# Kernel tuning notes

Measured on AMD Instinct MI355X. Metric: run time of the kernel, lower is better.

Reference implementation:

```python
import jax, jax.numpy as jnp
import numpy as np

KSIZE = 7
STRIDE = 4
SCALE = 10.0
C_IN = 64
C_INT = 16
TOP_M = 100


def _unfold(x, k, s):
    # x: [B,C,H,W] -> [B, C*k*k, L] with torch.nn.Unfold channel ordering (c, ki, kj)
    B, C, H, W = x.shape
    oh = (H - k) // s + 1
    ow = (W - k) // s + 1
    rows = jnp.arange(oh)[:, None] * s + jnp.arange(k)[None, :]  # [oh,k]
    cols = jnp.arange(ow)[:, None] * s + jnp.arange(k)[None, :]  # [ow,k]
    p = x[:, :, rows][:, :, :, :, cols]          # [B,C,oh,k,ow,k]
    p = p.transpose(0, 1, 3, 5, 2, 4)            # [B,C,k,k,oh,ow]
    return p.reshape(B, C * k * k, oh * ow)


def _fold(p, H, W, k, s):
    # inverse of _unfold with overlap-add (torch.nn.Fold semantics)
    B, D, L = p.shape
    C = D // (k * k)
    oh = (H - k) // s + 1
    ow = (W - k) // s + 1
    rows = jnp.arange(oh)[:, None] * s + jnp.arange(k)[None, :]
    cols = jnp.arange(ow)[:, None] * s + jnp.arange(k)[None, :]
    p = p.reshape(B, C, k, k, oh, ow).transpose(0, 1, 4, 2, 5, 3)  # [B,C,oh,k,ow,k]
    out = jnp.zeros((B, C, H, W), p.dtype)
    return out.at[:, :, rows[:, :, None, None], cols[None, None, :, :]].add(p)


def _conv1x1(x, w, b):
    return jnp.einsum('bchw,oc->bohw', x, w) + b[None, :, None, None]


def _conv3x3(x, w, b):
    y = jax.lax.conv_general_dilated(x, w, (1, 1), ((1, 1), (1, 1)),
                                     dimension_numbers=('NCHW', 'OIHW', 'NCHW'))
    return y + b[None, :, None, None]


def setup_inputs() -> dict:
    key = jax.random.key(0)
    ks = jax.random.split(key, 12)
    B, H, W = 4, 127, 127
    s = 0.05  # small init std keeps softmax logits in a sane range
    return {
        'x': jax.random.normal(ks[0], (B, C_IN, H, W), jnp.float32),
        'g_w': jax.random.normal(ks[1], (C_INT, C_IN, 3, 3), jnp.float32) * s,
        'g_b': jnp.zeros((C_INT,), jnp.float32),
        'theta_w': jax.random.normal(ks[2], (C_INT, C_IN), jnp.float32) * s,
        'theta_b': jnp.zeros((C_INT,), jnp.float32),
        'phi_w': jax.random.normal(ks[3], (C_INT, C_IN), jnp.float32) * s,
        'phi_b': jnp.zeros((C_INT,), jnp.float32),
        'match_w': jax.random.normal(ks[4], (C_INT, C_IN), jnp.float32) * s,
        'match_b': jnp.zeros((C_INT,), jnp.float32),
        'restore_w': jax.random.normal(ks[5], (C_IN, C_INT), jnp.float32) * s,
        'restore_b': jnp.zeros((C_IN,), jnp.float32),
    }


def reference(x, g_w, g_b, theta_w, theta_b, phi_w, phi_b,
              match_w, match_b, restore_w, restore_b):
    B, C, H, W = x.shape
    b1 = _conv3x3(x, g_w, g_b)           # [B,16,H,W]
    b2 = _conv1x1(x, theta_w, theta_b)
    b3 = _conv1x1(x, phi_w, phi_b)

    p1 = _unfold(b1, KSIZE, STRIDE).transpose(0, 2, 1)  # [B,L,D], D=16*49
    p2 = _unfold(b2, KSIZE, STRIDE).transpose(0, 2, 1)
    p3 = _unfold(b3, KSIZE, STRIDE).transpose(0, 2, 1)

    score = jnp.einsum('bld,bmd->blm', p1, p2)           # [B,L,L]
    L = score.shape[-1]
    k = min(TOP_M, L)
    vals, idx = jax.lax.top_k(score, k)                  # [B,L,k]
    bI = jnp.arange(B)[:, None, None]
    rI = jnp.arange(L)[None, :, None]
    sparse = jnp.zeros_like(score).at[bI, rI, idx].set(vals)
    attn = jax.nn.softmax(sparse * SCALE, axis=-1)

    agg = jnp.einsum('blm,bmd->bld', attn, p3).transpose(0, 2, 1)  # [B,D,L]
    out = _fold(agg, H, W, KSIZE, STRIDE)                # [B,16,H,W]

    mask = _fold(_unfold(jnp.ones_like(x), KSIZE, STRIDE), H, W, KSIZE, STRIDE)
    mask = _conv1x1(mask, match_w, match_b)              # [B,16,H,W]

    out = out / (mask + 1e-8)
    out = _conv1x1(out, restore_w, restore_b)            # [B,64,H,W]
    return out
```

## Files before the change

### kernel.cpp

```cpp
#include <hip/hip_runtime.h>
#include <hip/hip_bf16.h>

typedef __hip_bfloat16 bf16;
typedef unsigned short ushort_t;
typedef __attribute__((ext_vector_type(8))) __bf16 bfv8;
typedef __attribute__((ext_vector_type(16))) float f32x16;

#define B_   4
#define CIN  64
#define CI   16
#define H_   127
#define W_   127
#define HW   (H_*W_)
#define KS   7
#define ST   4
#define OH_  31
#define L_   961
#define D_   784
#define TOPM 100

#define N1   1032256
#define WG_O 4
#define WT_O (WG_O + 9216)
#define WP_O (WT_O + 1024)
#define BG_O (WP_O + 1024)
#define BT_O (BG_O + 16)
#define BP_O (BT_O + 16)
#define SM_O (BP_O + 16)
#define SB_O (SM_O + 16)
#define RW_O (SB_O + 16)
#define RB_O (RW_O + 1024)
#define B1_O 12448
#define S3_O (B1_O + 3*N1)
#define WB_O (S3_O + B_*D_)
#define REG_O (WB_O + 36864)
#define XHSZ 4129024
#define SROW 964
#define SCSLOT 926464
#define AGSZ 753424
#define TKROW 112
#define SLST 72
#define PKPLANE 753424
#define PKSTR   1506848

#define FULL_BYTES ((size_t)(REG_O + XHSZ + 4*AGSZ) * 4)
#define MID_BYTES  ((size_t)(REG_O + XHSZ) * 4)

__device__ __forceinline__ float bf2f(bf16 v) { return __bfloat162float(v); }
__device__ __forceinline__ float bflo(unsigned u) { return __uint_as_float(u << 16); }
__device__ __forceinline__ float bfhi(unsigned u) { return __uint_as_float(u & 0xFFFF0000u); }

template <typename T> struct Ld;
template <> struct Ld<float> {
  static __device__ __forceinline__ float f(const void* p, int i) { return ((const float*)p)[i]; }
};
template <> struct Ld<bf16> {
  static __device__ __forceinline__ float f(const void* p, int i) { return bf2f(((const bf16*)p)[i]); }
};

__device__ __forceinline__ unsigned fmap(float f) {
  unsigned u = __float_as_uint(f);
  return (u & 0x80000000u) ? ~u : (u | 0x80000000u);
}
__device__ __forceinline__ float unfmap(unsigned kk) {
  unsigned u = (kk & 0x80000000u) ? (kk & 0x7fffffffu) : ~kk;
  return __uint_as_float(u);
}

__device__ __forceinline__ ushort_t f2bf(float x) {
  unsigned u = __float_as_uint(x);
  return (ushort_t)((u + 0x7FFFu + ((u >> 16) & 1u)) >> 16);
}
__device__ __forceinline__ void splitbf(float x, ushort_t& h, ushort_t& l) {
  h = f2bf(x);
  float hf = __uint_as_float(((unsigned)h) << 16);
  l = f2bf(x - hf);
}

__global__ void k_detect(const unsigned short* __restrict__ xh, int* __restrict__ flag) {
  int tid = threadIdx.x;
  int c = 0;
#pragma unroll
  for (int j = 0; j < 2; ++j) {
    unsigned u = xh[tid * 2 + j];
    unsigned e = (u >> 7) & 0xFF;
    if (e >= 134) c++;
  }
#pragma unroll
  for (int o = 32; o; o >>= 1) c += __shfl_down(c, o);
  if (tid == 0) *flag = (c >= 8) ? 1 : 0;
}

#define LDW(ptr, i) (f ? ((const float*)(ptr))[i] : bf2f(((const bf16*)(ptr))[i]))
__global__ __launch_bounds__(256) void k_prep(
    const int* __restrict__ flag,
    const void* g_w, const void* t_w, const void* p_w,
    const void* g_b, const void* t_b, const void* p_b,
    const void* m_w, const void* m_b, const void* r_w, const void* r_b,
    float* __restrict__ ws)
{
  int f = *flag;
  int gid = blockIdx.x * 256 + threadIdx.x;
  int gs = gridDim.x * 256;
  for (int i = gid; i < 9216; i += gs) {
    int o = i & 15, t = i >> 4, c = t & 63, tap = t >> 6;
    ws[WG_O + i] = LDW(g_w, (o * 64 + c) * 9 + tap);
  }
  for (int i = gid; i < 1024; i += gs) {
    int o = i & 15, c = i >> 4;
    ws[WT_O + i] = LDW(t_w, o * 64 + c);
    ws[WP_O + i] = LDW(p_w, o * 64 + c);
  }
  if (gid < 16) {
    ws[BG_O + gid] = LDW(g_b, gid);
    ws[BT_O + gid] = LDW(t_b, gid);
    ws[BP_O + gid] = LDW(p_b, gid);
    float s = 0.f;
    for (int c = 0; c < 64; ++c) s += LDW(m_w, gid * 64 + c);
    ws[SM_O + gid] = s;
    ws[SB_O + gid] = LDW(m_b, gid);
  }
  for (int i = gid; i < 1024; i += gs) ws[RW_O + i] = LDW(r_w, i);
  if (gid >= 64 && gid < 128) ws[RB_O + gid - 64] = LDW(r_b, gid - 64);
  ushort_t* wBh = (ushort_t*)(ws + WB_O);
  ushort_t* wBl = wBh + 9 * 64 * 64;
  for (int i = gid; i < 9 * 64 * 64; i += gs) {
    int c = i & 63, t = i >> 6, col = t & 63, tap = t >> 6;
    float v = 0.f;
    if (col < 16) v = LDW(g_w, (col * 64 + c) * 9 + tap);
    else if (col < 32) { if (tap == 4) v = LDW(t_w, (col - 16) * 64 + c); }
    else if (col < 48) { if (tap == 4) v = LDW(p_w, (col - 32) * 64 + c); }
    ushort_t h, l; splitbf(v, h, l);
    wBh[i] = h; wBl[i] = l;
  }
}

__global__ __launch_bounds__(256) void k_hwc(
    const int* __restrict__ flag, const void* __restrict__ x,
    ushort_t* __restrict__ xhh, ushort_t* __restrict__ xhl)
{
  __shared__ float tile[64][65];
  int pix0 = blockIdx.x * 64;
  int tid = threadIdx.x;
  int g = tid >> 6, p = tid & 63;
  int pix = pix0 + p;
  bool ok = pix < B_ * HW;
  int bb = ok ? pix / HW : 0;
  int r  = ok ? pix - bb * HW : 0;
  if (*flag) {
    const float* xf = (const float*)x;
    for (int c = g * 16; c < g * 16 + 16; ++c)
      tile[p][c] = ok ? xf[((size_t)bb * CIN + c) * HW + r] : 0.f;
  } else {
    const bf16* xb = (const bf16*)x;
    for (int c = g * 16; c < g * 16 + 16; ++c)
      tile[p][c] = ok ? bf2f(xb[((size_t)bb * CIN + c) * HW + r]) : 0.f;
  }
  __syncthreads();
  int c2 = tid & 63, pg = tid >> 6;
  for (int k = 0; k < 16; ++k) {
    int p2 = pg * 16 + k;
    int pix2 = pix0 + p2;
    if (pix2 < B_ * HW) {
      ushort_t h, l; splitbf(tile[p2][c2], h, l);
      xhh[(size_t)pix2 * 64 + c2] = h;
      xhl[(size_t)pix2 * 64 + c2] = l;
    }
  }
}

__global__ __launch_bounds__(256) void k_conv3(
    const float* __restrict__ ws,
    const ushort_t* __restrict__ xhh, const ushort_t* __restrict__ xhl,
    ushort_t* __restrict__ b1h, ushort_t* __restrict__ b1l,
    ushort_t* __restrict__ b2h, ushort_t* __restrict__ b2l,
    ushort_t* __restrict__ b3)
{
  __shared__ ushort_t sAh[128 * SLST], sAl[128 * SLST];
  __shared__ ushort_t sBh[64 * SLST],  sBl[64 * SLST];
  int bz = blockIdx.z;
  int px0 = blockIdx.x * 128;
  int tid = threadIdx.x, lane = tid & 63, wv = tid >> 6;

  int pix0 = px0 + lane, pix1 = px0 + lane + 64;
  bool pok0 = pix0 < HW, pok1 = pix1 < HW;
  int ph0 = pok0 ? pix0 / W_ : 0, pw0 = pok0 ? pix0 - ph0 * W_ : 0;
  int ph1 = pok1 ? pix1 / W_ : 0, pw1 = pok1 ? pix1 - ph1 * W_ : 0;
  const ushort_t* xplane = ((wv == 0) ? xhh : xhl) + (size_t)bz * HW * 64;
  const ushort_t* wBh_ = (const ushort_t*)(ws + WB_O);
  const ushort_t* bsrc = (wv == 2) ? wBh_ : (wBh_ + 9 * 64 * 64);
  ushort_t* dplane = (wv == 0) ? sAh : (wv == 1) ? sAl : (wv == 2) ? sBh : sBl;
  ushort_t* drow0 = dplane + lane * SLST;
  ushort_t* drow1 = dplane + (lane + 64) * SLST;

  int fr = lane & 31, kh = (lane >> 5) << 3;
  int mt = (wv >> 1) << 1;
  int aoff0 = (mt * 32 + fr) * SLST + kh;
  int aoff1 = ((mt + 1) * 32 + fr) * SLST + kh;
  int boff  = (((wv & 1) << 5) + fr) * SLST + kh;

  f32x16 acc0 = {0.f,0.f,0.f,0.f,0.f,0.f,0.f,0.f,0.f,0.f,0.f,0.f,0.f,0.f,0.f,0.f};
  f32x16 acc1 = {0.f,0.f,0.f,0.f,0.f,0.f,0.f,0.f,0.f,0.f,0.f,0.f,0.f,0.f,0.f,0.f};
  const int4 z4 = make_int4(0, 0, 0, 0);
  int4 v0 = z4, v1 = z4, v2 = z4, v3 = z4, v4 = z4, v5 = z4, v6 = z4, v7 = z4;
  int4 u0 = z4, u1 = z4, u2 = z4, u3 = z4, u4 = z4, u5 = z4, u6 = z4, u7 = z4;

  if (wv < 2) {
    int hh = ph0 - 1, ww = pw0 - 1;
    if (pok0 && hh >= 0 && ww >= 0) {
      const int4* s = (const int4*)(xplane + (size_t)(hh * W_ + ww) * 64);
      v0 = s[0]; v1 = s[1]; v2 = s[2]; v3 = s[3]; v4 = s[4]; v5 = s[5]; v6 = s[6]; v7 = s[7];
    }
    int hh1 = ph1 - 1, ww1 = pw1 - 1;
    if (pok1 && hh1 >= 0 && ww1 >= 0) {
      const int4* s = (const int4*)(xplane + (size_t)(hh1 * W_ + ww1) * 64);
      u0 = s[0]; u1 = s[1]; u2 = s[2]; u3 = s[3]; u4 = s[4]; u5 = s[5]; u6 = s[6]; u7 = s[7];
    }
  } else {
    const int4* s = (const int4*)(bsrc + (size_t)lane * 64);
    v0 = s[0]; v1 = s[1]; v2 = s[2]; v3 = s[3]; v4 = s[4]; v5 = s[5]; v6 = s[6]; v7 = s[7];
  }

  for (int r = 0; r < 9; ++r) {
    __syncthreads();
    *(int4*)(drow0 + 0)  = v0;  *(int4*)(drow0 + 8)  = v1;
    *(int4*)(drow0 + 16) = v2;  *(int4*)(drow0 + 24) = v3;
    *(int4*)(drow0 + 32) = v4;  *(int4*)(drow0 + 40) = v5;
    *(int4*)(drow0 + 48) = v6;  *(int4*)(drow0 + 56) = v7;
    if (wv < 2) {
      *(int4*)(drow1 + 0)  = u0;  *(int4*)(drow1 + 8)  = u1;
      *(int4*)(drow1 + 16) = u2;  *(int4*)(drow1 + 24) = u3;
      *(int4*)(drow1 + 32) = u4;  *(int4*)(drow1 + 40) = u5;
      *(int4*)(drow1 + 48) = u6;  *(int4*)(drow1 + 56) = u7;
    }
    __syncthreads();
    if (r < 8) {
      int rn = r + 1;
      int dh = rn / 3 - 1, dw = rn % 3 - 1;
      if (wv < 2) {
        int hh = ph0 + dh, ww = pw0 + dw;
        if (pok0 && (unsigned)hh < (unsigned)H_ && (unsigned)ww < (unsigned)W_) {
          const int4* s = (const int4*)(xplane + (size_t)(hh * W_ + ww) * 64);
          v0 = s[0]; v1 = s[1]; v2 = s[2]; v3 = s[3]; v4 = s[4]; v5 = s[5]; v6 = s[6]; v7 = s[7];
        } else {
          v0 = z4; v1 = z4; v2 = z4; v3 = z4; v4 = z4; v5 = z4; v6 = z4; v7 = z4;
        }
        int hh1 = ph1 + dh, ww1 = pw1 + dw;
        if (pok1 && (unsigned)hh1 < (unsigned)H_ && (unsigned)ww1 < (unsigned)W_) {
          const int4* s = (const int4*)(xplane + (size_t)(hh1 * W_ + ww1) * 64);
          u0 = s[0]; u1 = s[1]; u2 = s[2]; u3 = s[3]; u4 = s[4]; u5 = s[5]; u6 = s[6]; u7 = s[7];
        } else {
          u0 = z4; u1 = z4; u2 = z4; u3 = z4; u4 = z4; u5 = z4; u6 = z4; u7 = z4;
        }
      } else {
        const int4* s = (const int4*)(bsrc + ((size_t)rn * 64 + lane) * 64);
        v0 = s[0]; v1 = s[1]; v2 = s[2]; v3 = s[3]; v4 = s[4]; v5 = s[5]; v6 = s[6]; v7 = s[7];
      }
    }
#pragma unroll
    for (int t = 0; t < 4; ++t) {
      bfv8 ah0 = *(const bfv8*)(sAh + aoff0 + t * 16);
      bfv8 al0 = *(const bfv8*)(sAl + aoff0 + t * 16);
      bfv8 ah1 = *(const bfv8*)(sAh + aoff1 + t * 16);
      bfv8 al1 = *(const bfv8*)(sAl + aoff1 + t * 16);
      bfv8 bh  = *(const bfv8*)(sBh + boff + t * 16);
      bfv8 bl  = *(const bfv8*)(sBl + boff + t * 16);
      acc0 = __builtin_amdgcn_mfma_f32_32x32x16_bf16(al0, bh, acc0, 0, 0, 0);
      acc0 = __builtin_amdgcn_mfma_f32_32x32x16_bf16(ah0, bl, acc0, 0, 0, 0);
      acc0 = __builtin_amdgcn_mfma_f32_32x32x16_bf16(ah0, bh, acc0, 0, 0, 0);
      acc1 = __builtin_amdgcn_mfma_f32_32x32x16_bf16(al1, bh, acc1, 0, 0, 0);
      acc1 = __builtin_amdgcn_mfma_f32_32x32x16_bf16(ah1, bl, acc1, 0, 0, 0);
      acc1 = __builtin_amdgcn_mfma_f32_32x32x16_bf16(ah1, bh, acc1, 0, 0, 0);
    }
  }

  int nw = ((wv & 1) << 5) + fr;
#pragma unroll
  for (int s = 0; s < 2; ++s) {
    int mbase = (mt + s) * 32;
#pragma unroll
    for (int r = 0; r < 16; ++r) {
      int m = mbase + (r & 3) + ((r >> 2) << 3) + ((lane >> 5) << 2);
      int p2 = px0 + m;
      if (p2 >= HW) continue;
      size_t ob = ((size_t)bz * HW + p2) * 16;
      float val = s ? acc1[r] : acc0[r];
      if (nw < 16) {
        ushort_t h2, l2; splitbf(val + ws[BG_O + nw], h2, l2);
        b1h[ob + nw] = h2; b1l[ob + nw] = l2;
      } else if (nw < 32) {
        int o = nw - 16; ushort_t h2, l2; splitbf(val + ws[BT_O + o], h2, l2);
        b2h[ob + o] = h2; b2l[ob + o] = l2;
      } else if (nw < 48) {
        int o = nw - 32; b3[ob + o] = f2bf(val + ws[BP_O + o]);
      }
    }
  }
}

template <typename T>
__device__ __forceinline__ void convF_body(
    const void* x, const void* g_w, const void* g_b,
    const void* t_w, const void* t_b, const void* p_w, const void* p_b,
    ushort_t* b1h, ushort_t* b1l, ushort_t* b2h, ushort_t* b2l, ushort_t* b3,
    float* sgw, float* stw, float* spw)
{
  int tid = threadIdx.y * 32 + threadIdx.x;
  for (int i = tid; i < CI * CIN * 9; i += 256) sgw[i] = Ld<T>::f(g_w, i);
  for (int i = tid; i < CI * CIN; i += 256) { stw[i] = Ld<T>::f(t_w, i); spw[i] = Ld<T>::f(p_w, i); }
  __syncthreads();

  int w = blockIdx.x * 32 + threadIdx.x;
  int h = blockIdx.y * 8 + threadIdx.y;
  int b = blockIdx.z;
  if (w >= W_ || h >= H_) return;

  float a1[CI], a2[CI], a3[CI];
#pragma unroll
  for (int o = 0; o < CI; ++o) { a1[o] = 0.f; a2[o] = 0.f; a3[o] = 0.f; }

  const size_t xb = (size_t)b * CIN * HW;
  for (int c = 0; c < CIN; ++c) {
    float xv[9];
#pragma unroll
    for (int dh = 0; dh < 3; ++dh) {
      int hh = h + dh - 1;
      bool rok = ((unsigned)hh < (unsigned)H_);
#pragma unroll
      for (int dw = 0; dw < 3; ++dw) {
        int ww = w + dw - 1;
        bool ok = rok && ((unsigned)ww < (unsigned)W_);
        xv[dh * 3 + dw] = ok ? Ld<T>::f(x, (int)(xb + (size_t)c * HW + hh * W_ + ww)) : 0.f;
      }
    }
    float xc = xv[4];
#pragma unroll
    for (int o = 0; o < CI; ++o) {
      const float* gg = &sgw[(o * CIN + c) * 9];
      float s = gg[0]*xv[0] + gg[1]*xv[1] + gg[2]*xv[2]
              + gg[3]*xv[3] + gg[4]*xv[4] + gg[5]*xv[5]
              + gg[6]*xv[6] + gg[7]*xv[7] + gg[8]*xv[8];
      a1[o] += s;
      a2[o] += stw[o * CIN + c] * xc;
      a3[o] += spw[o * CIN + c] * xc;
    }
  }
  size_t base = ((size_t)b * HW + h * W_ + w) * CI;
#pragma unroll
  for (int o = 0; o < CI; ++o) {
    float v1 = a1[o] + Ld<T>::f(g_b, o);
    float v2 = a2[o] + Ld<T>::f(t_b, o);
    ushort_t hh2, ll2;
    splitbf(v1, hh2, ll2); b1h[base + o] = hh2; b1l[base + o] = ll2;
    splitbf(v2, hh2, ll2); b2h[base + o] = hh2; b2l[base + o] = ll2;
    b3[base + o] = f2bf(a3[o] + Ld<T>::f(p_b, o));
  }
}

__global__ __launch_bounds__(256) void k_convF(
    const int* __restrict__ flag, const void* x,
    const void* g_w, const void* g_b, const void* t_w, const void* t_b,
    const void* p_w, const void* p_b,
    ushort_t* __restrict__ b1h, ushort_t* __restrict__ b1l,
    ushort_t* __restrict__ b2h, ushort_t* __restrict__ b2l,
    ushort_t* __restrict__ b3)
{
  __shared__ float sgw[CI * CIN * 9];
  __shared__ float stw[CI * CIN];
  __shared__ float spw[CI * CIN];
  if (*flag) convF_body<float>(x, g_w, g_b, t_w, t_b, p_w, p_b, b1h, b1l, b2h, b2l, b3, sgw, stw, spw);
  else       convF_body<bf16 >(x, g_w, g_b, t_w, t_b, p_w, p_b, b1h, b1l, b2h, b2l, b3, sgw, stw, spw);
}

__global__ __launch_bounds__(256) void k_colsum(const ushort_t* __restrict__ b3, float* __restrict__ S3)
{
  __shared__ float red[16][17];
  int b = blockIdx.x, pos = blockIdx.y;
  int ki = pos / 7, kj = pos % 7;
  int c = threadIdx.x & 15, chunk = threadIdx.x >> 4;
  const ushort_t* B3 = b3 + (size_t)b * HW * CI;
  float s = 0.f;
  for (int l = chunk; l < L_; l += 16) {
    int lh = l / OH_, lw = l % OH_;
    s += bflo((unsigned)B3[((lh * ST + ki) * W_ + lw * ST + kj) * CI + c]);
  }
  red[chunk][c] = s;
  __syncthreads();
  if (threadIdx.x < 16) {
    float t = 0.f;
#pragma unroll
    for (int k = 0; k < 16; ++k) t += red[k][threadIdx.x];
    S3[(b * 49 + pos) * 16 + threadIdx.x] = t;
  }
}

__global__ __launch_bounds__(256) void k_pack(
    const ushort_t* __restrict__ b1h, const ushort_t* __restrict__ b1l,
    ushort_t* __restrict__ pk, int b0, unsigned pkstride_z)
{
  int idx = blockIdx.x * 256 + threadIdx.x;
  if (idx >= 961 * 98) return;
  int row = idx / 98, rem = idx - row * 98;
  int nki = rem / 14, q = rem - nki * 14;
  int slh = row / OH_, slw = row - slh * OH_;
  int src = ((slh * ST) * W_ + slw * ST + nki * W_) * 16 + q * 8;
  int dst = (nki * 961 + row) * 112 + q * 8;
  int batch = b0 + blockIdx.y;
  size_t poff = (size_t)batch * HW * CI;
  ushort_t* pkb = pk + (size_t)blockIdx.y * pkstride_z;
  *(int4*)(pkb + dst)           = *(const int4*)(b1h + poff + src);
  *(int4*)(pkb + PKPLANE + dst) = *(const int4*)(b1l + poff + src);
}

__global__ __launch_bounds__(256) void k_score(
    const ushort_t* __restrict__ b2h, const ushort_t* __restrict__ b2l,
    const ushort_t* __restrict__ pk,
    float* __restrict__ scb, int b0, unsigned scstride_z, unsigned pkstride_z)
{
  __shared__ ushort_t sAh[128 * SLST], sAl[128 * SLST];
  __shared__ ushort_t sBh[64 * SLST],  sBl[64 * SLST];
  int batch = b0 + blockIdx.z;
  size_t poff_g = (size_t)batch * HW * CI;
  float* Sc = scb + (size_t)blockIdx.z * scstride_z;

  int tid = threadIdx.x;
  int m0 = blockIdx.y * 128, n0 = blockIdx.x * 64;
  int lane = tid & 63;
  int wv = tid >> 6;
  int grp = lane >> 3, ch = lane & 7;

  const ushort_t* pkb = pk + (size_t)blockIdx.z * pkstride_z + (size_t)(wv & 1) * PKPLANE;

  int srow = n0 + lane;  if (srow > L_ - 1) srow = L_ - 1;
  int slh = srow / OH_, slw = srow - slh * OH_;
  int sbase = (slh * ST) * W_ + slw * ST;
  const ushort_t* splane = (wv == 2) ? (b2h + poff_g) : (b2l + poff_g);
  ushort_t* dplane = (wv == 0) ? sAh : (wv == 1) ? sAl : (wv == 2) ? sBh : sBl;
  ushort_t* drowB = dplane + lane * SLST;

  int fr = lane & 31;
  int kh = (lane >> 5) << 3;
  int mt = (wv >> 1) << 1;
  int aoff0 = (mt * 32 + fr) * SLST + kh;
  int aoff1 = ((mt + 1) * 32 + fr) * SLST + kh;
  int boff  = (((wv & 1) << 5) + fr) * SLST + kh;

  f32x16 acc0 = {0.f,0.f,0.f,0.f,0.f,0.f,0.f,0.f,0.f,0.f,0.f,0.f,0.f,0.f,0.f,0.f};
  f32x16 acc1 = {0.f,0.f,0.f,0.f,0.f,0.f,0.f,0.f,0.f,0.f,0.f,0.f,0.f,0.f,0.f,0.f};

  int4 pv0, pv1, pv2, pv3, pv4, pv5, pv6, pv7;
  int4 pv8, pv9, pv10, pv11, pv12, pv13, pv14, pv15;

#define LA(j) pv##j = *(const int4*)(pks + (size_t)min(m0 + 8*j + grp, 960) * 112)
#define LA_ALL LA(0); LA(1); LA(2); LA(3); LA(4); LA(5); LA(6); LA(7); \
               LA(8); LA(9); LA(10); LA(11); LA(12); LA(13); LA(14); LA(15)
#define WA(j) *(int4*)(d0 + (j) * 8 * SLST) = pv##j
#define WA_ALL WA(0); WA(1); WA(2); WA(3); WA(4); WA(5); WA(6); WA(7); \
               WA(8); WA(9); WA(10); WA(11); WA(12); WA(13); WA(14); WA(15)

  if (wv < 2) {
    const ushort_t* pks = pkb + ch * 8;
    LA_ALL;
  } else {
    const int4* s0 = (const int4*)(splane + (size_t)sbase * 16);
    pv0 = s0[0]; pv1 = s0[1]; pv2 = s0[2]; pv3 = s0[3];
    pv4 = s0[4]; pv5 = s0[5]; pv6 = s0[6]; pv7 = s0[7];
  }

  for (int r = 0; r < 14; ++r) {
    int half = r & 1;
    __syncthreads();
    if (wv < 2) {
      ushort_t* d0 = dplane + grp * SLST + ch * 8;
      if (!half) { WA_ALL; }
      else if (ch < 6) { WA_ALL; }
    } else {
      *(int4*)(drowB + 0)  = pv0;  *(int4*)(drowB + 8)  = pv1;
      *(int4*)(drowB + 16) = pv2;  *(int4*)(drowB + 24) = pv3;
      *(int4*)(drowB + 32) = pv4;  *(int4*)(drowB + 40) = pv5;
      if (!half) { *(int4*)(drowB + 48) = pv6; *(int4*)(drowB + 56) = pv7; }
    }
    __syncthreads();
    if (r < 13) {
      int rn = r + 1;
      int nki = rn >> 1, odd = rn & 1;
      if (wv < 2) {
        const ushort_t* pks = pkb + (size_t)nki * (961 * 112) + odd * 64 + ch * 8;
        if (!odd) { LA_ALL; }
        else if (ch < 6) { LA_ALL; }
      } else {
        int nkj0 = odd * 4;
        const int4* s0 = (const int4*)(splane + (size_t)(sbase + nki * W_ + nkj0) * 16);
        pv0 = s0[0]; pv1 = s0[1]; pv2 = s0[2]; pv3 = s0[3]; pv4 = s0[4]; pv5 = s0[5];
        if (!odd) { pv6 = s0[6]; pv7 = s0[7]; }
      }
    }
    if (!half) {
#pragma unroll
      for (int t = 0; t < 4; ++t) {
        bfv8 ah0 = *(const bfv8*)(sAh + aoff0 + t * 16);
        bfv8 al0 = *(const bfv8*)(sAl + aoff0 + t * 16);
        bfv8 ah1 = *(const bfv8*)(sAh + aoff1 + t * 16);
        bfv8 al1 = *(const bfv8*)(sAl + aoff1 + t * 16);
        bfv8 bh  = *(const bfv8*)(sBh + boff + t * 16);
        bfv8 bl  = *(const bfv8*)(sBl + boff + t * 16);
        acc0 = __builtin_amdgcn_mfma_f32_32x32x16_bf16(al0, bh, acc0, 0, 0, 0);
        acc0 = __builtin_amdgcn_mfma_f32_32x32x16_bf16(ah0, bl, acc0, 0, 0, 0);
        acc0 = __builtin_amdgcn_mfma_f32_32x32x16_bf16(ah0, bh, acc0, 0, 0, 0);
        acc1 = __builtin_amdgcn_mfma_f32_32x32x16_bf16(al1, bh, acc1, 0, 0, 0);
        acc1 = __builtin_amdgcn_mfma_f32_32x32x16_bf16(ah1, bl, acc1, 0, 0, 0);
        acc1 = __builtin_amdgcn_mfma_f32_32x32x16_bf16(ah1, bh, acc1, 0, 0, 0);
      }
    } else {
#pragma unroll
      for (int t = 0; t < 3; ++t) {
        bfv8 ah0 = *(const bfv8*)(sAh + aoff0 + t * 16);
        bfv8 al0 = *(const bfv8*)(sAl + aoff0 + t * 16);
        bfv8 ah1 = *(const bfv8*)(sAh + aoff1 + t * 16);
        bfv8 al1 = *(const bfv8*)(sAl + aoff1 + t * 16);
        bfv8 bh  = *(const bfv8*)(sBh + boff + t * 16);
        bfv8 bl  = *(const bfv8*)(sBl + boff + t * 16);
        acc0 = __builtin_amdgcn_mfma_f32_32x32x16_bf16(al0, bh, acc0, 0, 0, 0);
        acc0 = __builtin_amdgcn_mfma_f32_32x32x16_bf16(ah0, bl, acc0, 0, 0, 0);
        acc0 = __builtin_amdgcn_mfma_f32_32x32x16_bf16(ah0, bh, acc0, 0, 0, 0);
        acc1 = __builtin_amdgcn_mfma_f32_32x32x16_bf16(al1, bh, acc1, 0, 0, 0);
        acc1 = __builtin_amdgcn_mfma_f32_32x32x16_bf16(ah1, bl, acc1, 0, 0, 0);
        acc1 = __builtin_amdgcn_mfma_f32_32x32x16_bf16(ah1, bh, acc1, 0, 0, 0);
      }
    }
  }
#undef LA
#undef LA_ALL
#undef WA
#undef WA_ALL

  int nw = n0 + ((wv & 1) << 5) + fr;
  if (nw < L_) {
    int mw0 = m0 + mt * 32;
#pragma unroll
    for (int r = 0; r < 16; ++r) {
      int m = mw0 + (r & 3) + ((r >> 2) << 3) + ((lane >> 5) << 2);
      if (m < L_) Sc[(size_t)m * SROW + nw] = acc0[r];
    }
    int mw1 = m0 + (mt + 1) * 32;
#pragma unroll
    for (int r = 0; r < 16; ++r) {
      int m = mw1 + (r & 3) + ((r >> 2) << 3) + ((lane >> 5) << 2);
      if (m < L_) Sc[(size_t)m * SROW + nw] = acc1[r];
    }
  }
}

__global__ __launch_bounds__(256) void k_topk(
    const float* __restrict__ scb, float* __restrict__ tkw, int* __restrict__ tkp,
    unsigned scstride_z)
{
  __shared__ float swv[4][TOPM];
  __shared__ int spx[4][TOPM];
  int tid = threadIdx.x;
  int wvi = tid >> 6, lane = tid & 63;
  int l = blockIdx.x * 4 + wvi;
  if (l > L_ - 1) l = L_ - 1;
  int bz = blockIdx.y;
  const float4* row4 = (const float4*)(scb + (size_t)bz * scstride_z + (size_t)l * SROW);
  int trow = (bz * L_ + l) * TKROW;

  unsigned k[16];
#pragma unroll
  for (int q = 0; q < 4; ++q) {
    float4 v = row4[q * 64 + lane];
    int ib = (q * 64 + lane) * 4;
    k[q * 4 + 0] = (ib + 0 < L_) ? fmap(v.x) : 0u;
    k[q * 4 + 1] = (ib + 1 < L_) ? fmap(v.y) : 0u;
    k[q * 4 + 2] = (ib + 2 < L_) ? fmap(v.z) : 0u;
    k[q * 4 + 3] = (ib + 3 < L_) ? fmap(v.w) : 0u;
  }

  unsigned mk = 0;
#pragma unroll
  for (int r = 0; r < 16; ++r) mk = max(mk, k[r]);
#pragma unroll
  for (int o = 32; o; o >>= 1) mk = max(mk, (unsigned)__shfl_down((int)mk, o));
  mk = (unsigned)__shfl((int)mk, 0);
  float vmax = unfmap(mk);

  unsigned kk[16];
#pragma unroll
  for (int r = 0; r < 16; ++r) kk[r] = k[r];

  unsigned prefix = 0; int base = 0;
  for (int bit = 30; bit >= 0; bit -= 2) {
    int n3 = 0, n2 = 0, n1 = 0;
#pragma unroll
    for (int r = 0; r < 16; ++r) {
      unsigned f = (kk[r] >> bit) & 3u;
      n3 += (int)__popcll(__ballot(f == 3u));
      n2 += (int)__popcll(__ballot(f >= 2u));
      n1 += (int)__popcll(__ballot(f >= 1u));
    }
    unsigned ch;
    if (base + n3 >= TOPM) ch = 3;
    else if (base + n2 >= TOPM) { ch = 2; base += n3; }
    else if (base + n1 >= TOPM) { ch = 1; base += n2; }
    else { ch = 0; base += n1; }
    prefix |= ch << bit;
#pragma unroll
    for (int r = 0; r < 16; ++r) {
      unsigned f = (kk[r] >> bit) & 3u;
      kk[r] = (f == ch) ? kk[r] : 0u;
    }
  }
  int nA = base;
  int needT = TOPM - nA;

  int cA = 0, cT = 0;
#pragma unroll
  for (int r = 0; r < 16; ++r) { cA += (k[r] > prefix); cT += (k[r] == prefix); }
  int pk = cA | (cT << 16);
  int incl = pk;
#pragma unroll
  for (int o = 1; o < 64; o <<= 1) { int t = __shfl_up(incl, o); if (lane >= o) incl += t; }
  int excl = incl - pk;
  int tA = excl & 0xFFFF, tT = excl >> 16;

  float M = fmaxf(10.f * vmax, 0.f);
  float e0 = __expf(-M);
  float z = 0.f;
#pragma unroll
  for (int r = 0; r < 16; ++r) {
    unsigned kr = k[r];
    int slot = -1;
    if (kr > prefix) slot = tA++;
    else if (kr == prefix) { if (tT < needT) slot = nA + tT; tT++; }
    if (slot >= 0) {
      float v = unfmap(kr);
      float wv = __expf(10.f * v - M);
      swv[wvi][slot] = wv; z += wv;
      int gi = 256 * (r >> 2) + 4 * lane + (r & 3);
      int lh = gi / OH_, lw = gi - lh * OH_;
      spx[wvi][slot] = ((lh * ST) * W_ + lw * ST) * CI;
    }
  }
#pragma unroll
  for (int o = 32; o; o >>= 1) z += __shfl_down(z, o);
  z = __shfl(z, 0);
  float Z = z + (float)(L_ - TOPM) * e0;
  float invZ = 1.f / Z;
  float w0 = e0 / Z;
  __syncthreads();
#pragma unroll
  for (int s0 = 0; s0 < 2; ++s0) {
    int s = lane + 64 * s0;
    if (s < TOPM) {
      tkw[trow + s] = swv[wvi][s] * invZ - w0;
      tkp[trow + s] = spx[wvi][s];
    }
  }
  if (lane == 0) tkw[trow + TOPM] = w0;
}

__global__ __launch_bounds__(128) void k_pv(
    const float* __restrict__ tkw, const int* __restrict__ tkp,
    const ushort_t* __restrict__ b3, const float* __restrict__ s3,
    float* __restrict__ agb, int b0, unsigned agstride_z)
{
  int l = blockIdx.x, bz = blockIdx.y;
  int batch = b0 + bz;
  int trow = (bz * L_ + l) * TKROW;
  const ushort_t* B3 = b3 + (size_t)batch * HW * CI;
  const float* S3 = s3 + (size_t)batch * D_;
  float* agg = agb + (size_t)bz * agstride_z;
  int tid = threadIdx.x;
  if (tid >= 98) return;

  float w0 = tkw[trow + TOPM];
  int pos = tid >> 1;
  int c0 = (tid & 1) << 3;
  int ki = pos / 7, kj = pos - (pos / 7) * 7;
  int poff = (ki * W_ + kj) * CI + c0;

  float a0 = 0.f, a1 = 0.f, a2 = 0.f, a3 = 0.f;
  float a4 = 0.f, a5 = 0.f, a6 = 0.f, a7 = 0.f;
  for (int j0 = 0; j0 < TOPM; j0 += 4) {
    float w_0 = tkw[trow + j0 + 0];
    float w_1 = tkw[trow + j0 + 1];
    float w_2 = tkw[trow + j0 + 2];
    float w_3 = tkw[trow + j0 + 3];
    int p_0 = tkp[trow + j0 + 0];
    int p_1 = tkp[trow + j0 + 1];
    int p_2 = tkp[trow + j0 + 2];
    int p_3 = tkp[trow + j0 + 3];
    const uint4 q0 = *(const uint4*)(B3 + p_0 + poff);
    const uint4 q1 = *(const uint4*)(B3 + p_1 + poff);
    const uint4 q2 = *(const uint4*)(B3 + p_2 + poff);
    const uint4 q3 = *(const uint4*)(B3 + p_3 + poff);
    a0 += w_0 * bflo(q0.x); a1 += w_0 * bfhi(q0.x); a2 += w_0 * bflo(q0.y); a3 += w_0 * bfhi(q0.y);
    a4 += w_0 * bflo(q0.z); a5 += w_0 * bfhi(q0.z); a6 += w_0 * bflo(q0.w); a7 += w_0 * bfhi(q0.w);
    a0 += w_1 * bflo(q1.x); a1 += w_1 * bfhi(q1.x); a2 += w_1 * bflo(q1.y); a3 += w_1 * bfhi(q1.y);
    a4 += w_1 * bflo(q1.z); a5 += w_1 * bfhi(q1.z); a6 += w_1 * bflo(q1.w); a7 += w_1 * bfhi(q1.w);
    a0 += w_2 * bflo(q2.x); a1 += w_2 * bfhi(q2.x); a2 += w_2 * bflo(q2.y); a3 += w_2 * bfhi(q2.y);
    a4 += w_2 * bflo(q2.z); a5 += w_2 * bfhi(q2.z); a6 += w_2 * bflo(q2.w); a7 += w_2 * bfhi(q2.w);
    a0 += w_3 * bflo(q3.x); a1 += w_3 * bfhi(q3.x); a2 += w_3 * bflo(q3.y); a3 += w_3 * bfhi(q3.y);
    a4 += w_3 * bflo(q3.z); a5 += w_3 * bfhi(q3.z); a6 += w_3 * bflo(q3.w); a7 += w_3 * bfhi(q3.w);
  }
  const float4 s40 = *(const float4*)(S3 + tid * 8);
  const float4 s41 = *(const float4*)(S3 + tid * 8 + 4);
  a0 += w0 * s40.x; a1 += w0 * s40.y; a2 += w0 * s40.z; a3 += w0 * s40.w;
  a4 += w0 * s41.x; a5 += w0 * s41.y; a6 += w0 * s41.z; a7 += w0 * s41.w;
  float* dst = agg + (size_t)l * D_ + tid * 8;
  *(float4*)(dst)     = make_float4(a0, a1, a2, a3);
  *(float4*)(dst + 4) = make_float4(a4, a5, a6, a7);
}

__global__ __launch_bounds__(256) void k_fold(
    const int* __restrict__ flag, const float* __restrict__ ws,
    const float* __restrict__ agb, void* __restrict__ out,
    int b0, unsigned agstride_z)
{
  __shared__ float srw[CIN * CI];
  int tid = threadIdx.x;
  for (int i = tid; i < CIN * CI; i += 256) srw[i] = ws[RW_O + i];
  __syncthreads();

  int bz = blockIdx.y;
  int batch = b0 + bz;
  const float* agg = agb + (size_t)bz * agstride_z;

  int gid = blockIdx.x * 256 + tid;
  if (gid >= HW) return;
  int h = gid / W_;
  int w = gid % W_;

  int lh0 = (h >= KS - 1) ? ((h - (KS - 1) + (ST - 1)) >> 2) : 0;
  int lh1 = min(OH_ - 1, h >> 2);
  int lw0 = (w >= KS - 1) ? ((w - (KS - 1) + (ST - 1)) >> 2) : 0;
  int lw1 = min(OH_ - 1, w >> 2);

  float t[CI];
#pragma unroll
  for (int c = 0; c < CI; ++c) t[c] = 0.f;
  for (int lh = lh0; lh <= lh1; ++lh) {
    int ki = h - ST * lh;
    for (int lw = lw0; lw <= lw1; ++lw) {
      int kj = w - ST * lw;
      const float* pb = agg + (size_t)(lh * OH_ + lw) * D_ + (ki * KS + kj) * CI;
      float4 q0 = *(const float4*)(pb);
      float4 q1 = *(const float4*)(pb + 4);
      float4 q2 = *(const float4*)(pb + 8);
      float4 q3 = *(const float4*)(pb + 12);
      t[0] += q0.x; t[1] += q0.y; t[2] += q0.z; t[3] += q0.w;
      t[4] += q1.x; t[5] += q1.y; t[6] += q1.z; t[7] += q1.w;
      t[8] += q2.x; t[9] += q2.y; t[10] += q2.z; t[11] += q2.w;
      t[12] += q3.x; t[13] += q3.y; t[14] += q3.z; t[15] += q3.w;
    }
  }
  float cnt = (float)((lh1 - lh0 + 1) * (lw1 - lw0 + 1));
  float r[CI];
#pragma unroll
  for (int c = 0; c < CI; ++c) r[c] = t[c] / (cnt * ws[SM_O + c] + ws[SB_O + c] + 1e-8f);

  size_t ob = (size_t)batch * CIN * HW + (size_t)h * W_ + w;
  if (*flag) {
    float* of = (float*)out;
#pragma unroll
    for (int o = 0; o < CIN; ++o) {
      float s = ws[RB_O + o];
#pragma unroll
      for (int c = 0; c < CI; ++c) s += srw[o * CI + c] * r[c];
      of[ob + (size_t)o * HW] = s;
    }
  } else {
    bf16* of = (bf16*)out;
#pragma unroll
    for (int o = 0; o < CIN; ++o) {
      float s = ws[RB_O + o];
#pragma unroll
      for (int c = 0; c < CI; ++c) s += srw[o * CI + c] * r[c];
      of[ob + (size_t)o * HW] = __float2bfloat16(s);
    }
  }
}

extern "C" void kernel_launch(void* const* d_in, const int* in_sizes, int n_in,
                              void* d_out, int out_size, void* d_ws, size_t ws_size,
                              hipStream_t stream)
{
  const void* x    = d_in[0];
  const void* g_w  = d_in[1];
  const void* g_b  = d_in[2];
  const void* th_w = d_in[3];
  const void* th_b = d_in[4];
  const void* ph_w = d_in[5];
  const void* ph_b = d_in[6];
  const void* m_w  = d_in[7];
  const void* m_b  = d_in[8];
  const void* r_w  = d_in[9];
  const void* r_b  = d_in[10];

  float* W = (float*)d_ws;
  int* flag = (int*)d_ws;
  ushort_t* planes = (ushort_t*)(W + B1_O);
  ushort_t* b1h = planes;
  ushort_t* b1l = planes + (size_t)N1;
  ushort_t* b2h = planes + (size_t)2 * N1;
  ushort_t* b2l = planes + (size_t)3 * N1;
  ushort_t* b3  = planes + (size_t)4 * N1;
  float* s3 = W + S3_O;

  k_detect<<<1, 64, 0, stream>>>((const unsigned short*)x, flag);
  k_prep<<<64, 256, 0, stream>>>(flag, g_w, th_w, ph_w, g_b, th_b, ph_b,
                                 m_w, m_b, r_w, r_b, W);

  if (ws_size >= FULL_BYTES) {
    ushort_t* xhh = (ushort_t*)(W + REG_O);
    ushort_t* xhl = xhh + (size_t)XHSZ;
    float* sc = W + REG_O;
    float* ag = W + REG_O + XHSZ;
    ushort_t* pk = (ushort_t*)ag;
    float* tkw = W + B1_O + N1;
    int*   tkp = (int*)(W + B1_O + N1 + N1 / 2);
    k_hwc<<<dim3((B_ * HW + 63) / 64), 256, 0, stream>>>(flag, x, xhh, xhl);
    k_conv3<<<dim3((HW + 127) / 128, 1, B_), 256, 0, stream>>>(
        W, xhh, xhl, b1h, b1l, b2h, b2l, b3);
    k_pack<<<dim3(368, B_), 256, 0, stream>>>(b1h, b1l, pk, 0, PKSTR);
    k_colsum<<<dim3(B_, 49), 256, 0, stream>>>(b3, s3);
    k_score<<<dim3(16, 8, B_), 256, 0, stream>>>(b2h, b2l, pk, sc, 0, SCSLOT, PKSTR);
    k_topk<<<dim3((L_ + 3) / 4, B_), 256, 0, stream>>>(sc, tkw, tkp, SCSLOT);
    k_pv<<<dim3(L_, B_), 128, 0, stream>>>(tkw, tkp, b3, s3, ag, 0, AGSZ);
    k_fold<<<dim3(64, B_), 256, 0, stream>>>(flag, W, ag, d_out, 0, AGSZ);
  } else if (ws_size >= MID_BYTES) {
    ushort_t* xhh = (ushort_t*)(W + REG_O);
    ushort_t* xhl = xhh + (size_t)XHSZ;
    float* sc = W + REG_O;
    float* ag = W + REG_O + SCSLOT;
    ushort_t* pk = (ushort_t*)ag;
    k_hwc<<<dim3((B_ * HW + 63) / 64), 256, 0, stream>>>(flag, x, xhh, xhl);
    k_conv3<<<dim3((HW + 127) / 128, 1, B_), 256, 0, stream>>>(
        W, xhh, xhl, b1h, b1l, b2h, b2l, b3);
    k_colsum<<<dim3(B_, 49), 256, 0, stream>>>(b3, s3);
    for (int b = 0; b < B_; ++b) {
      float* tkw = W + B1_O + N1 + (size_t)b * (HW * CI / 2);
      int*   tkp = (int*)(W + B1_O + N1 + N1 / 2 + (size_t)b * (HW * CI / 2));
      k_pack<<<dim3(368, 1), 256, 0, stream>>>(b1h, b1l, pk, b, 0);
      k_score<<<dim3(16, 8, 1), 256, 0, stream>>>(b2h, b2l, pk, sc, b, 0, 0);
      k_topk<<<dim3((L_ + 3) / 4, 1), 256, 0, stream>>>(sc, tkw, tkp, 0);
      k_pv<<<dim3(L_, 1), 128, 0, stream>>>(tkw, tkp, b3, s3, ag, b, 0);
      k_fold<<<dim3(64, 1), 256, 0, stream>>>(flag, W, ag, d_out, b, 0);
    }
  } else {
    float* sc = W + REG_O;
    float* ag = W + REG_O + SCSLOT;
    ushort_t* pk = (ushort_t*)ag;
    k_convF<<<dim3(4, 16, B_), dim3(32, 8, 1), 0, stream>>>(
        flag, x, g_w, g_b, th_w, th_b, ph_w, ph_b, b1h, b1l, b2h, b2l, b3);
    k_colsum<<<dim3(B_, 49), 256, 0, stream>>>(b3, s3);
    for (int b = 0; b < B_; ++b) {
      float* tkw = W + B1_O + N1 + (size_t)b * (HW * CI / 2);
      int*   tkp = (int*)(W + B1_O + N1 + N1 / 2 + (size_t)b * (HW * CI / 2));
      k_pack<<<dim3(368, 1), 256, 0, stream>>>(b1h, b1l, pk, b, 0);
      k_score<<<dim3(16, 8, 1), 256, 0, stream>>>(b2h, b2l, pk, sc, b, 0, 0);
      k_topk<<<dim3((L_ + 3) / 4, 1), 256, 0, stream>>>(sc, tkw, tkp, 0);
      k_pv<<<dim3(L_, 1), 128, 0, stream>>>(tkw, tkp, b3, s3, ag, b, 0);
      k_fold<<<dim3(64, 1), 256, 0, stream>>>(flag, W, ag, d_out, b, 0);
    }
  }
}
```

Baseline: 270.7 us.

## Use zero-padded HWC input and row-aligned tiles in the 3x3 conv kernel

The split-bf16 HWC copy of the input now goes into a buffer padded to 129x129 per image, and a new small kernel zeroes its border. The MFMA conv kernel then processes one image row per block and loads every tap without bounds checks or per-pixel division. This removes the branching and zero-fill logic from the conv inner loop. In exchange it adds a kernel launch, changes the workspace size thresholds, and leaves some MFMA rows unused because each tile covers 127 of 128 slots.

```diff
diff --git a/kernel.cpp b/kernel.cpp
--- a/kernel.cpp
+++ b/kernel.cpp
@@ -42,9 +42,13 @@
 #define SLST 72
 #define PKPLANE 753424
 #define PKSTR   1506848
+#define PADW 129
+#define PADPIX (PADW*PADW)
+#define XPB  (PADPIX*64)
+#define XPU  ((size_t)B_ * XPB)
 
 #define FULL_BYTES ((size_t)(REG_O + XHSZ + 4*AGSZ) * 4)
-#define MID_BYTES  ((size_t)(REG_O + XHSZ) * 4)
+#define MID_BYTES  ((size_t)(REG_O + 4260096) * 4)
 
 __device__ __forceinline__ float bf2f(bf16 v) { return __bfloat162float(v); }
 __device__ __forceinline__ float bflo(unsigned u) { return __uint_as_float(u << 16); }
@@ -133,6 +137,24 @@
     ushort_t h, l; splitbf(v, h, l);
     wBh[i] = h; wBl[i] = l;
   }
+}
+
+__global__ __launch_bounds__(256) void k_zpad(ushort_t* __restrict__ xhh,
+                                              ushort_t* __restrict__ xhl)
+{
+  int idx = blockIdx.x * 256 + threadIdx.x;
+  if (idx >= B_ * 512 * 8) return;
+  int q = idx & 7, t = idx >> 3;
+  int bp = t & 511, bb = t >> 9;
+  int pp;
+  if (bp < 129) pp = bp;
+  else if (bp < 258) pp = 128 * PADW + (bp - 129);
+  else if (bp < 385) pp = (bp - 257) * PADW;
+  else pp = (bp - 384) * PADW + 128;
+  size_t off = ((size_t)bb * PADPIX + pp) * 64 + q * 8;
+  const int4 z = make_int4(0, 0, 0, 0);
+  *(int4*)(xhh + off) = z;
+  *(int4*)(xhl + off) = z;
 }
 
 __global__ __launch_bounds__(256) void k_hwc(
@@ -158,14 +180,17 @@
   }
   __syncthreads();
   int c2 = tid & 63, pg = tid >> 6;
+  int pix2 = pix0 + pg * 16;
+  int bb2 = pix2 / HW, r2 = pix2 - bb2 * HW;
+  int h2 = r2 / W_, w2 = r2 - h2 * W_;
   for (int k = 0; k < 16; ++k) {
-    int p2 = pg * 16 + k;
-    int pix2 = pix0 + p2;
-    if (pix2 < B_ * HW) {
-      ushort_t h, l; splitbf(tile[p2][c2], h, l);
-      xhh[(size_t)pix2 * 64 + c2] = h;
-      xhl[(size_t)pix2 * 64 + c2] = l;
-    }
+    if (pix2 + k < B_ * HW) {
+      ushort_t h, l; splitbf(tile[pg * 16 + k][c2], h, l);
+      size_t off = ((size_t)bb2 * PADPIX + (size_t)(h2 + 1) * PADW + (w2 + 1)) * 64 + c2;
+      xhh[off] = h;
+      xhl[off] = l;
+    }
+    if (++w2 == W_) { w2 = 0; if (++h2 == H_) { h2 = 0; ++bb2; } }
   }
 }
 
@@ -179,19 +204,14 @@
   __shared__ ushort_t sAh[128 * SLST], sAl[128 * SLST];
   __shared__ ushort_t sBh[64 * SLST],  sBl[64 * SLST];
   int bz = blockIdx.z;
-  int px0 = blockIdx.x * 128;
+  int h = blockIdx.x;
   int tid = threadIdx.x, lane = tid & 63, wv = tid >> 6;
-
-  int pix0 = px0 + lane, pix1 = px0 + lane + 64;
-  bool pok0 = pix0 < HW, pok1 = pix1 < HW;
-  int ph0 = pok0 ? pix0 / W_ : 0, pw0 = pok0 ? pix0 - ph0 * W_ : 0;
-  int ph1 = pok1 ? pix1 / W_ : 0, pw1 = pok1 ? pix1 - ph1 * W_ : 0;
-  const ushort_t* xplane = ((wv == 0) ? xhh : xhl) + (size_t)bz * HW * 64;
+  int grp = lane >> 3, ch = lane & 7;
+
+  const ushort_t* xplane = ((wv == 0) ? xhh : xhl) + (size_t)bz * XPB;
   const ushort_t* wBh_ = (const ushort_t*)(ws + WB_O);
   const ushort_t* bsrc = (wv == 2) ? wBh_ : (wBh_ + 9 * 64 * 64);
   ushort_t* dplane = (wv == 0) ? sAh : (wv == 1) ? sAl : (wv == 2) ? sBh : sBl;
-  ushort_t* drow0 = dplane + lane * SLST;
-  ushort_t* drow1 = dplane + (lane + 64) * SLST;
 
   int fr = lane & 31, kh = (lane >> 5) << 3;
   int mt = (wv >> 1) << 1;
@@ -201,60 +221,44 @@
 
   f32x16 acc0 = {0.f,0.f,0.f,0.f,0.f,0.f,0.f,0.f,0.f,0.f,0.f,0.f,0.f,0.f,0.f,0.f};
   f32x16 acc1 = {0.f,0.f,0.f,0.f,0.f,0.f,0.f,0.f,0.f,0.f,0.f,0.f,0.f,0.f,0.f,0.f};
-  const int4 z4 = make_int4(0, 0, 0, 0);
-  int4 v0 = z4, v1 = z4, v2 = z4, v3 = z4, v4 = z4, v5 = z4, v6 = z4, v7 = z4;
-  int4 u0 = z4, u1 = z4, u2 = z4, u3 = z4, u4 = z4, u5 = z4, u6 = z4, u7 = z4;
+
+  int4 pv0, pv1, pv2, pv3, pv4, pv5, pv6, pv7;
+  int4 pv8, pv9, pv10, pv11, pv12, pv13, pv14, pv15;
+
+#define LC(j) pv##j = *(const int4*)(src + (j) * 512)
+#define LC_A  LC(0); LC(1); LC(2); LC(3); LC(4); LC(5); LC(6); LC(7); \
+              LC(8); LC(9); LC(10); LC(11); LC(12); LC(13); LC(14); LC(15)
+#define LC_W  LC(0); LC(1); LC(2); LC(3); LC(4); LC(5); LC(6); LC(7)
+#define WC(j) *(int4*)(d0 + (j) * 8 * SLST) = pv##j
+#define WC_A  WC(0); WC(1); WC(2); WC(3); WC(4); WC(5); WC(6); WC(7); \
+              WC(8); WC(9); WC(10); WC(11); WC(12); WC(13); WC(14); WC(15)
+#define WC_W  WC(0); WC(1); WC(2); WC(3); WC(4); WC(5); WC(6); WC(7)
 
   if (wv < 2) {
-    int hh = ph0 - 1, ww = pw0 - 1;
-    if (pok0 && hh >= 0 && ww >= 0) {
-      const int4* s = (const int4*)(xplane + (size_t)(hh * W_ + ww) * 64);
-      v0 = s[0]; v1 = s[1]; v2 = s[2]; v3 = s[3]; v4 = s[4]; v5 = s[5]; v6 = s[6]; v7 = s[7];
-    }
-    int hh1 = ph1 - 1, ww1 = pw1 - 1;
-    if (pok1 && hh1 >= 0 && ww1 >= 0) {
-      const int4* s = (const int4*)(xplane + (size_t)(hh1 * W_ + ww1) * 64);
-      u0 = s[0]; u1 = s[1]; u2 = s[2]; u3 = s[3]; u4 = s[4]; u5 = s[5]; u6 = s[6]; u7 = s[7];
-    }
+    const ushort_t* src = xplane + (size_t)h * (PADW * 64) + grp * 64 + ch * 8;
+    LC_A;
   } else {
-    const int4* s = (const int4*)(bsrc + (size_t)lane * 64);
-    v0 = s[0]; v1 = s[1]; v2 = s[2]; v3 = s[3]; v4 = s[4]; v5 = s[5]; v6 = s[6]; v7 = s[7];
+    const ushort_t* src = bsrc + grp * 64 + ch * 8;
+    LC_W;
   }
 
   for (int r = 0; r < 9; ++r) {
     __syncthreads();
-    *(int4*)(drow0 + 0)  = v0;  *(int4*)(drow0 + 8)  = v1;
-    *(int4*)(drow0 + 16) = v2;  *(int4*)(drow0 + 24) = v3;
-    *(int4*)(drow0 + 32) = v4;  *(int4*)(drow0 + 40) = v5;
-    *(int4*)(drow0 + 48) = v6;  *(int4*)(drow0 + 56) = v7;
-    if (wv < 2) {
-      *(int4*)(drow1 + 0)  = u0;  *(int4*)(drow1 + 8)  = u1;
-      *(int4*)(drow1 + 16) = u2;  *(int4*)(drow1 + 24) = u3;
-      *(int4*)(drow1 + 32) = u4;  *(int4*)(drow1 + 40) = u5;
-      *(int4*)(drow1 + 48) = u6;  *(int4*)(drow1 + 56) = u7;
+    {
+      ushort_t* d0 = dplane + grp * SLST + ch * 8;
+      if (wv < 2) { WC_A; } else { WC_W; }
     }
     __syncthreads();
     if (r < 8) {
       int rn = r + 1;
       int dh = rn / 3 - 1, dw = rn % 3 - 1;
       if (wv < 2) {
-        int hh = ph0 + dh, ww = pw0 + dw;
-        if (pok0 && (unsigned)hh < (unsigned)H_ && (unsigned)ww < (unsigned)W_) {
-          const int4* s = (const int4*)(xplane + (size_t)(hh * W_ + ww) * 64);
-          v0 = s[0]; v1 = s[1]; v2 = s[2]; v3 = s[3]; v4 = s[4]; v5 = s[5]; v6 = s[6]; v7 = s[7];
-        } else {
-          v0 = z4; v1 = z4; v2 = z4; v3 = z4; v4 = z4; v5 = z4; v6 = z4; v7 = z4;
-        }
-        int hh1 = ph1 + dh, ww1 = pw1 + dw;
-        if (pok1 && (unsigned)hh1 < (unsigned)H_ && (unsigned)ww1 < (unsigned)W_) {
-          const int4* s = (const int4*)(xplane + (size_t)(hh1 * W_ + ww1) * 64);
-          u0 = s[0]; u1 = s[1]; u2 = s[2]; u3 = s[3]; u4 = s[4]; u5 = s[5]; u6 = s[6]; u7 = s[7];
-        } else {
-          u0 = z4; u1 = z4; u2 = z4; u3 = z4; u4 = z4; u5 = z4; u6 = z4; u7 = z4;
-        }
+        const ushort_t* src = xplane
+            + ((size_t)(h + 1 + dh) * PADW + (1 + dw)) * 64 + grp * 64 + ch * 8;
+        LC_A;
       } else {
-        const int4* s = (const int4*)(bsrc + ((size_t)rn * 64 + lane) * 64);
-        v0 = s[0]; v1 = s[1]; v2 = s[2]; v3 = s[3]; v4 = s[4]; v5 = s[5]; v6 = s[6]; v7 = s[7];
+        const ushort_t* src = bsrc + rn * 4096 + grp * 64 + ch * 8;
+        LC_W;
       }
     }
 #pragma unroll
@@ -273,6 +277,12 @@
       acc1 = __builtin_amdgcn_mfma_f32_32x32x16_bf16(ah1, bh, acc1, 0, 0, 0);
     }
   }
+#undef LC
+#undef LC_A
+#undef LC_W
+#undef WC
+#undef WC_A
+#undef WC_W
 
   int nw = ((wv & 1) << 5) + fr;
 #pragma unroll
@@ -281,8 +291,8 @@
 #pragma unroll
     for (int r = 0; r < 16; ++r) {
       int m = mbase + (r & 3) + ((r >> 2) << 3) + ((lane >> 5) << 2);
-      int p2 = px0 + m;
-      if (p2 >= HW) continue;
+      if (m >= W_) continue;
+      int p2 = h * W_ + m;
       size_t ob = ((size_t)bz * HW + p2) * 16;
       float val = s ? acc1[r] : acc0[r];
       if (nw < 16) {
@@ -813,14 +823,15 @@
 
   if (ws_size >= FULL_BYTES) {
     ushort_t* xhh = (ushort_t*)(W + REG_O);
-    ushort_t* xhl = xhh + (size_t)XHSZ;
+    ushort_t* xhl = xhh + XPU;
     float* sc = W + REG_O;
     float* ag = W + REG_O + XHSZ;
     ushort_t* pk = (ushort_t*)ag;
     float* tkw = W + B1_O + N1;
     int*   tkp = (int*)(W + B1_O + N1 + N1 / 2);
+    k_zpad<<<64, 256, 0, stream>>>(xhh, xhl);
     k_hwc<<<dim3((B_ * HW + 63) / 64), 256, 0, stream>>>(flag, x, xhh, xhl);
-    k_conv3<<<dim3((HW + 127) / 128, 1, B_), 256, 0, stream>>>(
+    k_conv3<<<dim3(H_, 1, B_), 256, 0, stream>>>(
         W, xhh, xhl, b1h, b1l, b2h, b2l, b3);
     k_pack<<<dim3(368, B_), 256, 0, stream>>>(b1h, b1l, pk, 0, PKSTR);
     k_colsum<<<dim3(B_, 49), 256, 0, stream>>>(b3, s3);
@@ -830,12 +841,13 @@
     k_fold<<<dim3(64, B_), 256, 0, stream>>>(flag, W, ag, d_out, 0, AGSZ);
   } else if (ws_size >= MID_BYTES) {
     ushort_t* xhh = (ushort_t*)(W + REG_O);
-    ushort_t* xhl = xhh + (size_t)XHSZ;
+    ushort_t* xhl = xhh + XPU;
     float* sc = W + REG_O;
     float* ag = W + REG_O + SCSLOT;
     ushort_t* pk = (ushort_t*)ag;
+    k_zpad<<<64, 256, 0, stream>>>(xhh, xhl);
     k_hwc<<<dim3((B_ * HW + 63) / 64), 256, 0, stream>>>(flag, x, xhh, xhl);
-    k_conv3<<<dim3((HW + 127) / 128, 1, B_), 256, 0, stream>>>(
+    k_conv3<<<dim3(H_, 1, B_), 256, 0, stream>>>(
         W, xhh, xhl, b1h, b1l, b2h, b2l, b3);
     k_colsum<<<dim3(B_, 49), 256, 0, stream>>>(b3, s3);
     for (int b = 0; b < B_; ++b) {
```

New measurement: 262.8 us. 2.9% less time.
